# Performance work log

Measured on AMD Instinct MI355X. Metric: run time of the kernel, lower is better.

Reference implementation:

```python
import jax, jax.numpy as jnp
import numpy as np

NUM_HEADS = 4   # num_heads init kwarg
KERNEL = 7      # kernel_size init kwarg
EPS = 1e-5      # nn.LayerNorm default eps


def setup_inputs() -> dict:
    key = jax.random.key(0)
    ks = jax.random.split(key, 6)
    C, depth = 128, 2
    x = jax.random.normal(ks[0], (2, C, 64, 64), jnp.float32)
    qkv_w = jax.random.normal(ks[1], (depth, 3 * C, C), jnp.float32) * 0.05
    qkv_b = jnp.zeros((depth, 3 * C), jnp.float32)
    rpb = jax.random.normal(ks[2], (depth, NUM_HEADS, 2 * KERNEL - 1, 2 * KERNEL - 1), jnp.float32) * 0.02
    proj_w = jax.random.normal(ks[3], (depth, C, C), jnp.float32) * 0.05
    proj_b = jnp.zeros((depth, C), jnp.float32)
    ln_g = jnp.ones((C,), jnp.float32)
    ln_b = jnp.zeros((C,), jnp.float32)
    return dict(x=x, qkv_w=qkv_w, qkv_b=qkv_b, rpb=rpb,
                proj_w=proj_w, proj_b=proj_b, ln_g=ln_g, ln_b=ln_b)


def _na2d(x, w_qkv, b_qkv, rpb, w_p, b_p):
    """NATTEN-style 2D neighborhood attention. x: (B,H,W,C)."""
    B, H, W, C = x.shape
    h, k = NUM_HEADS, KERNEL
    d = C // h
    qkv = (x @ w_qkv.T + b_qkv).reshape(B, H, W, 3, h, d)
    q = qkv[..., 0, :, :] * (d ** -0.5)   # (B,H,W,h,d)
    kk = qkv[..., 1, :, :]
    v = qkv[..., 2, :, :]
    # edge-clamped window starts: each query sees exactly k x k neighbors
    si = jnp.clip(jnp.arange(H) - k // 2, 0, H - k)
    sj = jnp.clip(jnp.arange(W) - k // 2, 0, W - k)
    idx_i = si[:, None] + jnp.arange(k)   # (H,k) absolute row indices
    idx_j = sj[:, None] + jnp.arange(k)   # (W,k) absolute col indices

    def win(t):  # (B,H,W,h,d) -> (B,H,W,k,k,h,d)
        t = t[:, idx_i]          # (B,H,k,W,h,d)
        t = t[:, :, :, idx_j]    # (B,H,k,W,k,h,d)
        return jnp.transpose(t, (0, 1, 3, 2, 4, 5, 6))

    kw = win(kk)
    vw = win(v)
    attn = jnp.einsum('bijhd,bijpqhd->bijhpq', q, kw)  # (B,H,W,h,k,k)
    # relative position bias: index = (neighbor_abs - query) + (k-1)
    bi = jnp.arange(k)[None, :] + (k - 1) - (jnp.arange(H) - si)[:, None]  # (H,k)
    bj = jnp.arange(k)[None, :] + (k - 1) - (jnp.arange(W) - sj)[:, None]  # (W,k)
    bias = rpb[:, bi[:, None, :, None], bj[None, :, None, :]]  # (h,H,W,k,k)
    attn = attn + jnp.transpose(bias, (1, 2, 0, 3, 4))[None]
    attn = jax.nn.softmax(attn.reshape(B, H, W, h, k * k), axis=-1).reshape(B, H, W, h, k, k)
    out = jnp.einsum('bijhpq,bijpqhd->bijhd', attn, vw).reshape(B, H, W, C)
    return out @ w_p.T + b_p


def reference(x, qkv_w, qkv_b, rpb, proj_w, proj_b, ln_g, ln_b):
    y = jnp.transpose(x, (0, 2, 3, 1))  # NCHW -> NHWC
    for l in range(qkv_w.shape[0]):     # depth=2 stacked NA layers
        y = _na2d(y, qkv_w[l], qkv_b[l], rpb[l], proj_w[l], proj_b[l])
    mu = y.mean(-1, keepdims=True)
    var = y.var(-1, keepdims=True)
    y = (y - mu) / jnp.sqrt(var + EPS) * ln_g + ln_b
    return jnp.transpose(y, (0, 3, 1, 2))  # NHWC -> NCHW
```

## Files before the change

### kernel.cpp

```cpp
#include <hip/hip_runtime.h>
#include <hip/hip_bf16.h>
#include <math.h>

#define PIX 8192
typedef __hip_bfloat16 bf16;
typedef __attribute__((ext_vector_type(8))) short short8;
typedef __attribute__((ext_vector_type(4))) float f32x4;

__device__ inline float bflo(unsigned u) { return __uint_as_float(u << 16); }
__device__ inline float bfhi(unsigned u) { return __uint_as_float(u & 0xffff0000u); }
__device__ inline unsigned short f2b(float f) {
  __hip_bfloat16 h = __float2bfloat16(f);
  return *reinterpret_cast<unsigned short*>(&h);
}
__device__ inline unsigned pack2(float a, float b) {
  return (unsigned)f2b(a) | ((unsigned)f2b(b) << 16);
}

__global__ __launch_bounds__(256) void cvtw(const float* __restrict__ qw,
                                            const float* __restrict__ pw,
                                            unsigned short* __restrict__ wq,
                                            unsigned short* __restrict__ wp) {
  int idx = blockIdx.x * 256 + threadIdx.x;
  if (idx < 98304) wq[idx] = f2b(qw[idx]);
  if (idx < 32768) wp[idx] = f2b(pw[idx]);
}

__global__ __launch_bounds__(256) void xqkv(const float* __restrict__ x,
                                            const unsigned short* __restrict__ wq,
                                            const float* __restrict__ qb,
                                            unsigned short* __restrict__ qkv) {
  __shared__ __align__(16) unsigned short As[16 * 136];
  int m0 = blockIdx.x * 16;
  int tid = threadIdx.x;
  int b = m0 >> 12, i = (m0 >> 6) & 63, j0 = m0 & 63;

  for (int idx = tid; idx < 2048; idx += 256) {
    int c = idx >> 4, jl = idx & 15;
    As[jl * 136 + c] =
        f2b(x[(size_t)b * 524288 + (size_t)c * 4096 + i * 64 + j0 + jl]);
  }
  __syncthreads();

  int w = tid >> 6, lane = tid & 63;
  int quad = lane >> 4, l16 = lane & 15;
  short8 a[4];
#pragma unroll
  for (int kc = 0; kc < 4; ++kc)
    a[kc] = *(const short8*)(As + l16 * 136 + kc * 32 + quad * 8);
#pragma unroll
  for (int nt = 0; nt < 6; ++nt) {
    int col = w * 96 + nt * 16 + l16;
    const short8* bp = (const short8*)(wq + (size_t)col * 128 + quad * 8);
    f32x4 c = {0.f, 0.f, 0.f, 0.f};
#pragma unroll
    for (int kc = 0; kc < 4; ++kc)
      c = __builtin_amdgcn_mfma_f32_16x16x32_bf16(a[kc], bp[kc * 4], c, 0, 0, 0);
    float bv = qb[col];
#pragma unroll
    for (int r2 = 0; r2 < 4; ++r2)
      qkv[(size_t)(m0 + quad * 4 + r2) * 384 + col] = f2b(c[r2] + bv);
  }
}

__global__ __launch_bounds__(256) void gemm_mfma(const unsigned short* __restrict__ A,
                                                 const unsigned short* __restrict__ W,
                                                 const float* __restrict__ bias,
                                                 unsigned short* __restrict__ Cmat,
                                                 int N) {
  int m0 = blockIdx.x * 64, n0 = blockIdx.y * 64;
  int tid = threadIdx.x;
  int w = tid >> 6, lane = tid & 63;
  int quad = lane >> 4, l16 = lane & 15;

  const short8* ap =
      (const short8*)(A + (size_t)(m0 + w * 16 + l16) * 128 + quad * 8);
  short8 a[4];
#pragma unroll
  for (int kc = 0; kc < 4; ++kc) a[kc] = ap[kc * 4];

  f32x4 acc[4];
#pragma unroll
  for (int nt = 0; nt < 4; ++nt) {
    const short8* bp =
        (const short8*)(W + (size_t)(n0 + nt * 16 + l16) * 128 + quad * 8);
    f32x4 c = {0.f, 0.f, 0.f, 0.f};
#pragma unroll
    for (int kc = 0; kc < 4; ++kc)
      c = __builtin_amdgcn_mfma_f32_16x16x32_bf16(a[kc], bp[kc * 4], c, 0, 0, 0);
    acc[nt] = c;
  }

#pragma unroll
  for (int nt = 0; nt < 4; ++nt) {
    int col = n0 + nt * 16 + l16;
    float bv = bias[col];
#pragma unroll
    for (int r = 0; r < 4; ++r) {
      int m = m0 + w * 16 + quad * 4 + r;
      Cmat[(size_t)m * N + col] = f2b(acc[nt][r] + bv);
    }
  }
}

#define RSTRIDE 72
__global__ __launch_bounds__(256, 2) void na_attn(const unsigned short* __restrict__ qkvp,
                                                  const float* __restrict__ rpb,
                                                  unsigned short* __restrict__ out) {
  __shared__ __align__(16) unsigned short kbuf[140 * RSTRIDE];
  __shared__ __align__(16) unsigned short vbuf[140 * RSTRIDE];
  __shared__ float rb[338];
  __shared__ float sc[64][52];

  int ti = blockIdx.x >> 4, tj = blockIdx.x & 15;
  int hp = blockIdx.y;
  int bz = blockIdx.z;
  int tid = threadIdx.x;
  int bi0 = ti * 8 - 3, bj0 = tj * 4 - 3;

  for (int t = tid; t < 338; t += 256) rb[t] = rpb[hp * 338 + t];

  for (int t = tid; t < 2240; t += 256) {
    int row = t >> 4;
    int sub = t & 15;
    int isv = sub >> 3;
    int c = sub & 7;
    int ri = row / 10, rj = row - ri * 10;
    int gi = bi0 + ri, gj = bj0 + rj;
    uint4 val = make_uint4(0, 0, 0, 0);
    if ((unsigned)gi < 64u && (unsigned)gj < 64u) {
      int pixn = (bz * 64 + gi) * 64 + gj;
      val = *(const uint4*)(qkvp + (size_t)pixn * 384 + 128 + isv * 128 +
                            hp * 64 + c * 8);
    }
    *(uint4*)((isv ? vbuf : kbuf) + row * RSTRIDE + c * 8) = val;
  }
  __syncthreads();

  int r = tid & 3;
  int hl = (tid >> 2) & 1;
  int px = tid >> 3;
  int ph = px * 2 + hl;
  int pi = px >> 2, pj = px & 3;
  int i = ti * 8 + pi, j = tj * 4 + pj;
  int si = min(max(i - 3, 0), 57), sj = min(max(j - 3, 0), 57);
  int li = si - bi0, lj = sj - bj0;
  int oi = i - si, oj = j - sj;
  int H = hp * 2 + hl;
  int pix = (bz * 64 + i) * 64 + j;

  const float scale = 0.17677669529663687f;
  float q[8];
  {
    uint4 t = *(const uint4*)(qkvp + (size_t)pix * 384 + H * 32 + r * 8);
    q[0] = bflo(t.x) * scale;  q[1] = bfhi(t.x) * scale;
    q[2] = bflo(t.y) * scale;  q[3] = bfhi(t.y) * scale;
    q[4] = bflo(t.z) * scale;  q[5] = bfhi(t.z) * scale;
    q[6] = bflo(t.w) * scale;  q[7] = bfhi(t.w) * scale;
  }

  const unsigned short* kh = kbuf + hl * 32 + r * 8;
  const unsigned short* vh = vbuf + hl * 32 + r * 8;
  const float* rbh = rb + hl * 169;

#pragma unroll
  for (int p = 0; p < 7; ++p) {
#pragma unroll
    for (int qq = 0; qq < 7; ++qq) {
      int n = (li + p) * 10 + (lj + qq);
      uint4 t = *(const uint4*)(kh + n * RSTRIDE);
      float dot = q[0] * bflo(t.x) + q[1] * bfhi(t.x)
                + q[2] * bflo(t.y) + q[3] * bfhi(t.y)
                + q[4] * bflo(t.z) + q[5] * bfhi(t.z)
                + q[6] * bflo(t.w) + q[7] * bfhi(t.w);
      dot += __shfl_xor(dot, 1);
      dot += __shfl_xor(dot, 2);
      if (r == 0) sc[ph][p * 7 + qq] = dot + rbh[(p + 6 - oi) * 13 + (qq + 6 - oj)];
    }
  }
  __syncthreads();

  float m = -INFINITY;
#pragma unroll
  for (int n = 0; n < 49; ++n) m = fmaxf(m, sc[ph][n]);

  float sum = 0.f;
  float acc[8] = {0.f, 0.f, 0.f, 0.f, 0.f, 0.f, 0.f, 0.f};
#pragma unroll
  for (int p = 0; p < 7; ++p) {
#pragma unroll
    for (int qq = 0; qq < 7; ++qq) {
      float e = __expf(sc[ph][p * 7 + qq] - m);
      sum += e;
      int n = (li + p) * 10 + (lj + qq);
      uint4 t = *(const uint4*)(vh + n * RSTRIDE);
      acc[0] += e * bflo(t.x);  acc[1] += e * bfhi(t.x);
      acc[2] += e * bflo(t.y);  acc[3] += e * bfhi(t.y);
      acc[4] += e * bflo(t.z);  acc[5] += e * bfhi(t.z);
      acc[6] += e * bflo(t.w);  acc[7] += e * bfhi(t.w);
    }
  }
  float inv = 1.f / sum;
  uint4 t;
  t.x = pack2(acc[0] * inv, acc[1] * inv);
  t.y = pack2(acc[2] * inv, acc[3] * inv);
  t.z = pack2(acc[4] * inv, acc[5] * inv);
  t.w = pack2(acc[6] * inv, acc[7] * inv);
  *(uint4*)(out + (size_t)pix * 128 + H * 32 + r * 8) = t;
}

__global__ __launch_bounds__(256) void ln_out(const unsigned short* __restrict__ y,
                                              const float* __restrict__ g,
                                              const float* __restrict__ bta,
                                              float* __restrict__ out) {
  __shared__ float tile[64][129];
  __shared__ float mean_s[64], rstd_s[64];
  int blk = blockIdx.x;
  int b = blk >> 6, i = blk & 63;
  int tid = threadIdx.x;
  const unsigned short* yrow = y + (size_t)blk * 64 * 128;
  for (int idx = tid; idx < 8192; idx += 256) {
    int j = idx >> 7, c = idx & 127;
    tile[j][c] = __uint_as_float((unsigned)yrow[idx] << 16);
  }
  __syncthreads();
  int jj = tid >> 2, qtr = tid & 3;
  float sum = 0.f, sumsq = 0.f;
#pragma unroll
  for (int cc = 0; cc < 32; ++cc) {
    float v = tile[jj][qtr * 32 + cc];
    sum += v; sumsq += v * v;
  }
  sum += __shfl_xor(sum, 1);  sum += __shfl_xor(sum, 2);
  sumsq += __shfl_xor(sumsq, 1);  sumsq += __shfl_xor(sumsq, 2);
  if (qtr == 0) {
    float mu = sum * (1.f / 128.f);
    mean_s[jj] = mu;
    rstd_s[jj] = rsqrtf(sumsq * (1.f / 128.f) - mu * mu + 1e-5f);
  }
  __syncthreads();
  int c0 = tid >> 6;
  int j = tid & 63;
  for (int c = c0; c < 128; c += 4) {
    float v = (tile[j][c] - mean_s[j]) * rstd_s[j] * g[c] + bta[c];
    out[(((size_t)b * 128 + c) * 64 + i) * 64 + j] = v;
  }
}

extern "C" void kernel_launch(void* const* d_in, const int* in_sizes, int n_in,
                              void* d_out, int out_size, void* d_ws, size_t ws_size,
                              hipStream_t stream) {
  (void)in_sizes; (void)n_in; (void)out_size; (void)ws_size;
  const float* x   = (const float*)d_in[0];
  const float* qw  = (const float*)d_in[1];
  const float* qb  = (const float*)d_in[2];
  const float* rpb = (const float*)d_in[3];
  const float* pw  = (const float*)d_in[4];
  const float* pb  = (const float*)d_in[5];
  const float* lg  = (const float*)d_in[6];
  const float* lb  = (const float*)d_in[7];

  unsigned short* y    = (unsigned short*)d_ws;
  unsigned short* qkv  = y + (size_t)PIX * 128;
  unsigned short* wq   = qkv + (size_t)PIX * 384;
  unsigned short* wp   = wq + 98304;
  unsigned short* attn = (unsigned short*)d_out;
  float* out = (float*)d_out;

  cvtw<<<384, 256, 0, stream>>>(qw, pw, wq, wp);
  xqkv<<<512, 256, 0, stream>>>(x, wq, qb, qkv);
  na_attn<<<dim3(128, 2, 2), 256, 0, stream>>>(qkv, rpb, attn);
  gemm_mfma<<<dim3(128, 2), 256, 0, stream>>>(attn, wp, pb, y, 128);
  gemm_mfma<<<dim3(128, 6), 256, 0, stream>>>(y, wq + 49152, qb + 384, qkv, 384);
  na_attn<<<dim3(128, 2, 2), 256, 0, stream>>>(qkv, rpb + 676, attn);
  gemm_mfma<<<dim3(128, 2), 256, 0, stream>>>(attn, wp + 16384, pb + 128, y, 128);
  ln_out<<<128, 256, 0, stream>>>(y, lg, lb, out);
}
```

Before: 146.6 us.

## Shrink attention tile to 4x4 pixels and split head dim over 8 lanes

The neighborhood attention kernel now handles 4x4 query pixels per block instead of 8x4, so the halo buffer shrinks to 10x10 and twice as many blocks are launched. Each head's 32-dim vector is now spread over 8 lanes with 4 elements each instead of 4 lanes with 8, using an extra shuffle step to reduce the dot product. Less shared memory and fewer registers per block allow occupancy of 4 blocks per CU and more parallelism. In exchange, halo K/V loads are redundant across more tiles, and there are extra shuffles and narrower memory accesses.

```diff
diff --git a/kernel.cpp b/kernel.cpp
--- a/kernel.cpp
+++ b/kernel.cpp
@@ -103,24 +103,24 @@
   }
 }
 
-#define RSTRIDE 72
-__global__ __launch_bounds__(256, 2) void na_attn(const unsigned short* __restrict__ qkvp,
+#define R7STRIDE 68
+__global__ __launch_bounds__(256, 4) void na_attn(const unsigned short* __restrict__ qkvp,
                                                   const float* __restrict__ rpb,
                                                   unsigned short* __restrict__ out) {
-  __shared__ __align__(16) unsigned short kbuf[140 * RSTRIDE];
-  __shared__ __align__(16) unsigned short vbuf[140 * RSTRIDE];
+  __shared__ __align__(16) unsigned short kbuf[100 * R7STRIDE];
+  __shared__ __align__(16) unsigned short vbuf[100 * R7STRIDE];
   __shared__ float rb[338];
-  __shared__ float sc[64][52];
+  __shared__ float sc[32][50];
 
   int ti = blockIdx.x >> 4, tj = blockIdx.x & 15;
   int hp = blockIdx.y;
   int bz = blockIdx.z;
   int tid = threadIdx.x;
-  int bi0 = ti * 8 - 3, bj0 = tj * 4 - 3;
+  int bi0 = ti * 4 - 3, bj0 = tj * 4 - 3;
 
   for (int t = tid; t < 338; t += 256) rb[t] = rpb[hp * 338 + t];
 
-  for (int t = tid; t < 2240; t += 256) {
+  for (int t = tid; t < 1600; t += 256) {
     int row = t >> 4;
     int sub = t & 15;
     int isv = sub >> 3;
@@ -133,16 +133,16 @@
       val = *(const uint4*)(qkvp + (size_t)pixn * 384 + 128 + isv * 128 +
                             hp * 64 + c * 8);
     }
-    *(uint4*)((isv ? vbuf : kbuf) + row * RSTRIDE + c * 8) = val;
-  }
-  __syncthreads();
-
-  int r = tid & 3;
-  int hl = (tid >> 2) & 1;
-  int px = tid >> 3;
+    *(uint4*)((isv ? vbuf : kbuf) + row * R7STRIDE + c * 8) = val;
+  }
+  __syncthreads();
+
+  int r = tid & 7;
+  int hl = (tid >> 3) & 1;
+  int px = tid >> 4;
   int ph = px * 2 + hl;
   int pi = px >> 2, pj = px & 3;
-  int i = ti * 8 + pi, j = tj * 4 + pj;
+  int i = ti * 4 + pi, j = tj * 4 + pj;
   int si = min(max(i - 3, 0), 57), sj = min(max(j - 3, 0), 57);
   int li = si - bi0, lj = sj - bj0;
   int oi = i - si, oj = j - sj;
@@ -150,17 +150,15 @@
   int pix = (bz * 64 + i) * 64 + j;
 
   const float scale = 0.17677669529663687f;
-  float q[8];
+  float q[4];
   {
-    uint4 t = *(const uint4*)(qkvp + (size_t)pix * 384 + H * 32 + r * 8);
+    uint2 t = *(const uint2*)(qkvp + (size_t)pix * 384 + H * 32 + r * 4);
     q[0] = bflo(t.x) * scale;  q[1] = bfhi(t.x) * scale;
     q[2] = bflo(t.y) * scale;  q[3] = bfhi(t.y) * scale;
-    q[4] = bflo(t.z) * scale;  q[5] = bfhi(t.z) * scale;
-    q[6] = bflo(t.w) * scale;  q[7] = bfhi(t.w) * scale;
-  }
-
-  const unsigned short* kh = kbuf + hl * 32 + r * 8;
-  const unsigned short* vh = vbuf + hl * 32 + r * 8;
+  }
+
+  const unsigned short* kh = kbuf + hl * 32 + r * 4;
+  const unsigned short* vh = vbuf + hl * 32 + r * 4;
   const float* rbh = rb + hl * 169;
 
 #pragma unroll
@@ -168,13 +166,12 @@
 #pragma unroll
     for (int qq = 0; qq < 7; ++qq) {
       int n = (li + p) * 10 + (lj + qq);
-      uint4 t = *(const uint4*)(kh + n * RSTRIDE);
+      uint2 t = *(const uint2*)(kh + n * R7STRIDE);
       float dot = q[0] * bflo(t.x) + q[1] * bfhi(t.x)
-                + q[2] * bflo(t.y) + q[3] * bfhi(t.y)
-                + q[4] * bflo(t.z) + q[5] * bfhi(t.z)
-                + q[6] * bflo(t.w) + q[7] * bfhi(t.w);
+                + q[2] * bflo(t.y) + q[3] * bfhi(t.y);
       dot += __shfl_xor(dot, 1);
       dot += __shfl_xor(dot, 2);
+      dot += __shfl_xor(dot, 4);
       if (r == 0) sc[ph][p * 7 + qq] = dot + rbh[(p + 6 - oi) * 13 + (qq + 6 - oj)];
     }
   }
@@ -185,7 +182,7 @@
   for (int n = 0; n < 49; ++n) m = fmaxf(m, sc[ph][n]);
 
   float sum = 0.f;
-  float acc[8] = {0.f, 0.f, 0.f, 0.f, 0.f, 0.f, 0.f, 0.f};
+  float acc[4] = {0.f, 0.f, 0.f, 0.f};
 #pragma unroll
   for (int p = 0; p < 7; ++p) {
 #pragma unroll
@@ -193,20 +190,16 @@
       float e = __expf(sc[ph][p * 7 + qq] - m);
       sum += e;
       int n = (li + p) * 10 + (lj + qq);
-      uint4 t = *(const uint4*)(vh + n * RSTRIDE);
+      uint2 t = *(const uint2*)(vh + n * R7STRIDE);
       acc[0] += e * bflo(t.x);  acc[1] += e * bfhi(t.x);
       acc[2] += e * bflo(t.y);  acc[3] += e * bfhi(t.y);
-      acc[4] += e * bflo(t.z);  acc[5] += e * bfhi(t.z);
-      acc[6] += e * bflo(t.w);  acc[7] += e * bfhi(t.w);
     }
   }
   float inv = 1.f / sum;
-  uint4 t;
+  uint2 t;
   t.x = pack2(acc[0] * inv, acc[1] * inv);
   t.y = pack2(acc[2] * inv, acc[3] * inv);
-  t.z = pack2(acc[4] * inv, acc[5] * inv);
-  t.w = pack2(acc[6] * inv, acc[7] * inv);
-  *(uint4*)(out + (size_t)pix * 128 + H * 32 + r * 8) = t;
+  *(uint2*)(out + (size_t)pix * 128 + H * 32 + r * 4) = t;
 }
 
 __global__ __launch_bounds__(256) void ln_out(const unsigned short* __restrict__ y,
@@ -269,10 +262,10 @@
 
   cvtw<<<384, 256, 0, stream>>>(qw, pw, wq, wp);
   xqkv<<<512, 256, 0, stream>>>(x, wq, qb, qkv);
-  na_attn<<<dim3(128, 2, 2), 256, 0, stream>>>(qkv, rpb, attn);
+  na_attn<<<dim3(256, 2, 2), 256, 0, stream>>>(qkv, rpb, attn);
   gemm_mfma<<<dim3(128, 2), 256, 0, stream>>>(attn, wp, pb, y, 128);
   gemm_mfma<<<dim3(128, 6), 256, 0, stream>>>(y, wq + 49152, qb + 384, qkv, 384);
-  na_attn<<<dim3(128, 2, 2), 256, 0, stream>>>(qkv, rpb + 676, attn);
+  na_attn<<<dim3(256, 2, 2), 256, 0, stream>>>(qkv, rpb + 676, attn);
   gemm_mfma<<<dim3(128, 2), 256, 0, stream>>>(attn, wp + 16384, pb + 128, y, 128);
   ln_out<<<128, 256, 0, stream>>>(y, lg, lb, out);
 }
```

Result: no change. 148.8 us (+1.5%).
